# Kernel optimization log

Measured on AMD Instinct MI355X. Metric: run time of the kernel, lower is better.

## Reference

```python
import jax, jax.numpy as jnp
import numpy as np
import math

B, ENC, SEQ, H = 32, 512, 1024, 8
HD = SEQ // H  # 128
EPS = 1e-5


def setup_inputs() -> dict:
    key = jax.random.key(0)
    ks = jax.random.split(key, 7)
    s = 0.02
    return {
        "x": jax.random.normal(ks[0], (B, ENC, SEQ), jnp.float32),
        "ln_g": jnp.ones((SEQ,), jnp.float32),
        "ln_b": jnp.zeros((SEQ,), jnp.float32),
        "w_in": jax.random.normal(ks[1], (3 * SEQ, SEQ), jnp.float32) * s,
        "b_in": jnp.zeros((3 * SEQ,), jnp.float32),
        "w_m1a": jax.random.normal(ks[2], (HD, HD), jnp.float32) * s,
        "b_m1a": jnp.zeros((HD,), jnp.float32),
        "w_m1b": jax.random.normal(ks[3], (1, HD), jnp.float32) * s,
        "b_m1b": jnp.zeros((1,), jnp.float32),
        "w_m2": jax.random.normal(ks[4], (1, ENC), jnp.float32) * s,
        "b_m2": jnp.zeros((1,), jnp.float32),
        "w_out": jax.random.normal(ks[5], (SEQ, 2 * SEQ), jnp.float32) * s,
        "b_out": jnp.zeros((SEQ,), jnp.float32),
    }


def reference(x, ln_g, ln_b, w_in, b_in, w_m1a, b_m1a, w_m1b, b_m1b,
              w_m2, b_m2, w_out, b_out):
    Bsz, N, S = x.shape  # N == enc_in, S == seq_len == d_model
    hd = S // H
    scale = 1.0 / math.sqrt(hd * N)

    # LayerNorm over last dim
    mu = jnp.mean(x, axis=-1, keepdims=True)
    var = jnp.mean(jnp.square(x - mu), axis=-1, keepdims=True)
    xn = (x - mu) * jax.lax.rsqrt(var + EPS) * ln_g + ln_b

    qkv = xn @ w_in.T + b_in  # [B, N, 3S]
    q, k, v = jnp.split(qkv, 3, axis=-1)
    # torch .view(B, H, N, hd) on contiguous [B, N, S] is a raw reshape
    q = q.reshape(Bsz, H, N, hd)
    k = k.reshape(Bsz, H, N, hd)
    v = v.reshape(Bsz, H, N, hd)

    def mlp1(t):  # [B,H,N,hd] -> [B,H,N]
        h1 = jnp.maximum(jnp.einsum('bhnd,ed->bhne', t, w_m1a) + b_m1a, 0.0)
        return jnp.einsum('bhne,e->bhn', h1, w_m1b[0]) + b_m1b[0]

    def mlp2(t):  # [B,H,N,hd] -> [B,H,hd] (Linear over N then ReLU)
        return jnp.maximum(jnp.einsum('bhnd,n->bhd', t, w_m2[0]) + b_m2[0], 0.0)

    # rank-1 outer-product scores, broadcast-multiplied into v
    s_qk = mlp1(q)[..., None] * mlp2(k)[:, :, None, :] * scale  # [B,H,N,hd]
    v1 = (s_qk * v).reshape(Bsz, N, S)
    s_kq = mlp1(k)[..., None] * mlp2(q)[:, :, None, :] * scale
    v2 = (s_kq * v).reshape(Bsz, N, S)

    out = jnp.concatenate([v1, v2], axis=-1) @ w_out.T + b_out  # [B,N,S]
    return out + x  # dropout is identity at eval
```

## Files before the change

kernel.cpp:

```cpp
#include <hip/hip_runtime.h>
#include <cstdint>
#include <cstddef>

#define BSZ   32
#define ENCN  512
#define SEQL  1024
#define MROWS (BSZ*ENCN)
#define N1    (3*SEQL)
#define K1    SEQL
#define N2    SEQL
#define K2    (2*SEQL)

typedef __bf16 bf16;
typedef __bf16 bf16x8 __attribute__((ext_vector_type(8)));
typedef __bf16 bf16x4 __attribute__((ext_vector_type(4)));
typedef float  f32x4  __attribute__((ext_vector_type(4)));
typedef int    i32x4  __attribute__((ext_vector_type(4)));
typedef int    i32x8  __attribute__((ext_vector_type(8)));

__device__ __forceinline__ void gl_lds16(const void* g, void* l) {
  __builtin_amdgcn_global_load_lds(
      (const __attribute__((address_space(1))) void*)(uintptr_t)g,
      (__attribute__((address_space(3))) void*)(uintptr_t)(uint32_t)(uintptr_t)l,
      16, 0, 0);
}

__device__ __forceinline__ f32x4 mfma16(bf16x8 a, bf16x8 b, f32x4 c) {
  return __builtin_amdgcn_mfma_f32_16x16x32_bf16(a, b, c, 0, 0, 0);
}

__device__ __forceinline__ uint32_t pk4_fp8(float a, float b, float c, float d) {
  int v = __builtin_amdgcn_cvt_pk_fp8_f32(a, b, 0, false);
  v = __builtin_amdgcn_cvt_pk_fp8_f32(c, d, v, true);
  return (uint32_t)v;
}

__global__ __launch_bounds__(256) void cvt_w_kernel(const float* __restrict__ w_in,
                                                    const float* __restrict__ w_out,
                                                    const float* __restrict__ w1a,
                                                    uint8_t* __restrict__ wi8,
                                                    uint8_t* __restrict__ wo8,
                                                    bf16* __restrict__ w1ab) {
  int idx = blockIdx.x * 256 + threadIdx.x;
  const int NWIN4 = (N1 * K1) / 4;
  const int NOUT4 = (N2 * K2) / 4;
  if (idx < NWIN4) {
    float4 v = ((const float4*)w_in)[idx];
    ((uint32_t*)wi8)[idx] = pk4_fp8(v.x * 64.f, v.y * 64.f, v.z * 64.f, v.w * 64.f);
  } else if (idx < NWIN4 + NOUT4) {
    int j = idx - NWIN4;
    float4 v = ((const float4*)w_out)[j];
    ((uint32_t*)wo8)[j] = pk4_fp8(v.x * 64.f, v.y * 64.f, v.z * 64.f, v.w * 64.f);
  } else {
    int j = idx - NWIN4 - NOUT4;
    float4 v = ((const float4*)w1a)[j];
    bf16x4 o = { (bf16)v.x, (bf16)v.y, (bf16)v.z, (bf16)v.w };
    ((bf16x4*)w1ab)[j] = o;
  }
}

__global__ __launch_bounds__(256) void ln_kernel(const float* __restrict__ x,
                                                 const float* __restrict__ g,
                                                 const float* __restrict__ bt,
                                                 uint8_t* __restrict__ xn8) {
  int row = blockIdx.x;
  int t = threadIdx.x;
  const float4 v = ((const float4*)(x + (size_t)row * SEQL))[t];
  float s  = v.x + v.y + v.z + v.w;
  float ss = v.x*v.x + v.y*v.y + v.z*v.z + v.w*v.w;
  for (int off = 32; off; off >>= 1) {
    s  += __shfl_down(s,  off, 64);
    ss += __shfl_down(ss, off, 64);
  }
  __shared__ float red[8];
  int w = t >> 6, l = t & 63;
  if (l == 0) { red[w] = s; red[w + 4] = ss; }
  __syncthreads();
  float st  = red[0] + red[1] + red[2] + red[3];
  float sst = red[4] + red[5] + red[6] + red[7];
  float mu   = st * (1.0f / SEQL);
  float var  = sst * (1.0f / SEQL) - mu * mu;
  float rstd = rsqrtf(var + 1e-5f);
  float4 gv = ((const float4*)g)[t];
  float4 bv = ((const float4*)bt)[t];
  float y0 = (v.x - mu) * rstd * gv.x + bv.x;
  float y1 = (v.y - mu) * rstd * gv.y + bv.y;
  float y2 = (v.z - mu) * rstd * gv.z + bv.z;
  float y3 = (v.w - mu) * rstd * gv.w + bv.w;
  ((uint32_t*)(xn8 + (size_t)row * SEQL))[t] = pk4_fp8(y0, y1, y2, y3);
}

template <int MODE, int SA, int SB>
__global__ __launch_bounds__(256) void gemm_fp8(const uint8_t* __restrict__ A,
                                                const uint8_t* __restrict__ Bw,
                                                const float* __restrict__ bias,
                                                const float* __restrict__ resid,
                                                void* __restrict__ Cout,
                                                int M, int N, int K) {
  __shared__ uint8_t Als[128 * 128];
  __shared__ uint8_t Bls[128 * 128];
  const int tid = threadIdx.x;
  const int w = tid >> 6, l = tid & 63;
  const int wm = w & 1, wn = w >> 1;
  const int q = l >> 4, li = l & 15;
  const int m0 = blockIdx.x * 128;
  const int n0 = blockIdx.y * 128;

  const int srow = tid >> 3;
  const int scol = ((tid & 7) ^ (srow & 7)) << 4;

  const int c0 = ((2 * q)     ^ (li & 7)) << 4;
  const int c1 = ((2 * q + 1) ^ (li & 7)) << 4;

  f32x4 acc[4][4] = {};

  for (int k0 = 0; k0 < K; k0 += 128) {
#pragma unroll
    for (int is = 0; is < 4; is++) {
      gl_lds16(A  + (size_t)(m0 + is * 32 + srow) * K + k0 + scol,
               (char*)Als + is * 4096 + w * 1024);
      gl_lds16(Bw + (size_t)(n0 + is * 32 + srow) * K + k0 + scol,
               (char*)Bls + is * 4096 + w * 1024);
    }
    __syncthreads();
    i32x8 af[4], bfg[4];
#pragma unroll
    for (int i = 0; i < 4; i++) {
      int r = wm * 64 + i * 16 + li;
      i32x4 lo = *(const i32x4*)&Als[r * 128 + c0];
      i32x4 hi = *(const i32x4*)&Als[r * 128 + c1];
      af[i] = i32x8{lo[0], lo[1], lo[2], lo[3], hi[0], hi[1], hi[2], hi[3]};
    }
#pragma unroll
    for (int j = 0; j < 4; j++) {
      int r = wn * 64 + j * 16 + li;
      i32x4 lo = *(const i32x4*)&Bls[r * 128 + c0];
      i32x4 hi = *(const i32x4*)&Bls[r * 128 + c1];
      bfg[j] = i32x8{lo[0], lo[1], lo[2], lo[3], hi[0], hi[1], hi[2], hi[3]};
    }
#pragma unroll
    for (int i = 0; i < 4; i++)
#pragma unroll
      for (int j = 0; j < 4; j++)
        acc[i][j] = __builtin_amdgcn_mfma_scale_f32_16x16x128_f8f6f4(
            af[i], bfg[j], acc[i][j], 0 , 0 ,
            0, SA, 0, SB);
    __syncthreads();
  }

#pragma unroll
  for (int i = 0; i < 4; i++)
#pragma unroll
    for (int j = 0; j < 4; j++) {
      int col = n0 + wn * 64 + j * 16 + li;
      float bv = bias[col];
#pragma unroll
      for (int r = 0; r < 4; r++) {
        int row = m0 + wm * 64 + i * 16 + q * 4 + r;
        float v = acc[i][j][r] + bv;
        if (MODE == 0) {
          ((bf16*)Cout)[(size_t)row * N + col] = (bf16)v;
        } else {
          ((float*)Cout)[(size_t)row * N + col] = v + resid[(size_t)row * N + col];
        }
      }
    }
}

__global__ __launch_bounds__(256) void mlp1_kernel(const bf16* __restrict__ qkv,
                                                   const bf16* __restrict__ w1ab,
                                                   const float* __restrict__ b1a,
                                                   const float* __restrict__ w1b,
                                                   const float* __restrict__ b1b,
                                                   float* __restrict__ A1q,
                                                   float* __restrict__ A1k) {
  const int bid = blockIdx.x;
  const int tensor = bid >> 10;
  const int mtile = bid & 1023;
  const int tid = threadIdx.x;
  const int w = tid >> 6, l = tid & 63;
  const int wm = w & 1, wn = w >> 1;
  const int q = l >> 4, li = l & 15;

  bf16x8 bfrag[4][4];
#pragma unroll
  for (int kq = 0; kq < 4; kq++)
#pragma unroll
    for (int j = 0; j < 4; j++) {
      int n = wn * 64 + j * 16 + li;
      bfrag[kq][j] = *(const bf16x8*)&w1ab[n * 128 + kq * 32 + q * 8];
    }

  f32x4 acc[4][4] = {};
#pragma unroll
  for (int kq = 0; kq < 4; kq++) {
#pragma unroll
    for (int i = 0; i < 4; i++) {
      int cg = mtile * 128 + wm * 64 + i * 16 + li;
      int b = cg >> 12;
      int c = cg & 4095;
      const bf16* ap = qkv + (size_t)(b * 512 + (c >> 3)) * N1
                           + tensor * 1024 + (c & 7) * 128 + kq * 32 + q * 8;
      bf16x8 af = *(const bf16x8*)ap;
#pragma unroll
      for (int j = 0; j < 4; j++)
        acc[i][j] = mfma16(af, bfrag[kq][j], acc[i][j]);
    }
  }

  float b1av[4], w1bv[4];
#pragma unroll
  for (int j = 0; j < 4; j++) {
    int col = wn * 64 + j * 16 + li;
    b1av[j] = b1a[col];
    w1bv[j] = w1b[col];
  }
  __shared__ float red[2][128];
  float p[4][4];
#pragma unroll
  for (int i = 0; i < 4; i++)
#pragma unroll
    for (int r = 0; r < 4; r++) {
      float s = 0.f;
#pragma unroll
      for (int j = 0; j < 4; j++) {
        float h = acc[i][j][r] + b1av[j];
        s += fmaxf(h, 0.f) * w1bv[j];
      }
      for (int off = 1; off < 16; off <<= 1) s += __shfl_xor(s, off, 64);
      p[i][r] = s;
    }
  if (li == 0) {
#pragma unroll
    for (int i = 0; i < 4; i++)
#pragma unroll
      for (int r = 0; r < 4; r++)
        red[wn][wm * 64 + i * 16 + q * 4 + r] = p[i][r];
  }
  __syncthreads();
  if (tid < 128) {
    float v = red[0][tid] + red[1][tid] + b1b[0];
    float* outp = tensor ? A1k : A1q;
    outp[mtile * 128 + tid] = v;
  }
}

__global__ __launch_bounds__(256) void mlp2_kernel(const bf16* __restrict__ qkv,
                                                   const float* __restrict__ w2,
                                                   const float* __restrict__ b2,
                                                   float* __restrict__ A2q,
                                                   float* __restrict__ A2k) {
  __shared__ float w2s[512];
  __shared__ float red[256][8];
  const int bid = blockIdx.x;
  const int tensor = bid >> 8;
  const int bh = bid & 255;
  const int b = bh >> 3, h = bh & 7;
  const int t = threadIdx.x;
  w2s[t] = w2[t];
  w2s[t + 256] = w2[t + 256];
  __syncthreads();

  const int half = t >> 7, cg = t & 127;
  const bf16* base = qkv + (size_t)(b * 512 + h * 64) * N1 + tensor * 1024 + cg * 8;
  float acc[8] = {0, 0, 0, 0, 0, 0, 0, 0};
  for (int rr = half; rr < 64; rr += 2) {
    bf16x8 v = *(const bf16x8*)(base + (size_t)rr * N1);
    float wn = w2s[rr * 8 + (cg >> 4)];
#pragma unroll
    for (int e = 0; e < 8; e++) acc[e] += (float)v[e] * wn;
  }
#pragma unroll
  for (int e = 0; e < 8; e++) red[t][e] = acc[e];
  __syncthreads();
  if (t < 128) {
    int m = t >> 3, e = t & 7;
    float s = 0.f;
#pragma unroll
    for (int a = 0; a < 8; a++)
      s += red[a * 16 + m][e] + red[128 + a * 16 + m][e];
    s += b2[0];
    float* o = tensor ? A2k : A2q;
    o[b * 1024 + h * 128 + t] = fmaxf(s, 0.f);
  }
}

__global__ __launch_bounds__(256) void scale_kernel(const bf16* __restrict__ qkv,
                                                    const float* __restrict__ A1q,
                                                    const float* __restrict__ A1k,
                                                    const float* __restrict__ A2q,
                                                    const float* __restrict__ A2k,
                                                    uint8_t* __restrict__ Y) {
  size_t idx = ((size_t)blockIdx.x * 256 + threadIdx.x) * 8;
  int b = (int)(idx >> 19);
  int f = (int)(idx & 524287);
  int chunk = f >> 7;
  float a1q = A1q[b * 4096 + chunk] * 64.f;
  float a1k = A1k[b * 4096 + chunk] * 64.f;
  int a2i = b * 1024 + ((f >> 16) << 7) + (f & 127);
  float4 k0 = *(const float4*)&A2k[a2i];
  float4 k1 = *(const float4*)&A2k[a2i + 4];
  float4 q0 = *(const float4*)&A2q[a2i];
  float4 q1 = *(const float4*)&A2q[a2i + 4];
  int row = b * 512 + (f >> 10);
  int col = f & 1023;
  bf16x8 v = *(const bf16x8*)&qkv[(size_t)row * N1 + 2048 + col];
  float kk[8] = { k0.x, k0.y, k0.z, k0.w, k1.x, k1.y, k1.z, k1.w };
  float qq[8] = { q0.x, q0.y, q0.z, q0.w, q1.x, q1.y, q1.z, q1.w };
  float y1[8], y2[8];
#pragma unroll
  for (int e = 0; e < 8; e++) {
    float vv = (float)v[e];
    y1[e] = a1q * kk[e] * vv;
    y2[e] = a1k * qq[e] * vv;
  }
  uint8_t* yr = Y + (size_t)row * K2;
  ((uint32_t*)(yr + col))[0] = pk4_fp8(y1[0], y1[1], y1[2], y1[3]);
  ((uint32_t*)(yr + col))[1] = pk4_fp8(y1[4], y1[5], y1[6], y1[7]);
  ((uint32_t*)(yr + 1024 + col))[0] = pk4_fp8(y2[0], y2[1], y2[2], y2[3]);
  ((uint32_t*)(yr + 1024 + col))[1] = pk4_fp8(y2[4], y2[5], y2[6], y2[7]);
}

extern "C" void kernel_launch(void* const* d_in, const int* in_sizes, int n_in,
                              void* d_out, int out_size, void* d_ws, size_t ws_size,
                              hipStream_t stream) {
  const float* x     = (const float*)d_in[0];
  const float* ln_g  = (const float*)d_in[1];
  const float* ln_b  = (const float*)d_in[2];
  const float* w_in  = (const float*)d_in[3];
  const float* b_in  = (const float*)d_in[4];
  const float* w1a   = (const float*)d_in[5];
  const float* b1a   = (const float*)d_in[6];
  const float* w1b   = (const float*)d_in[7];
  const float* b1b   = (const float*)d_in[8];
  const float* w2    = (const float*)d_in[9];
  const float* b2    = (const float*)d_in[10];
  const float* w_out = (const float*)d_in[11];
  const float* b_out = (const float*)d_in[12];
  float* out = (float*)d_out;
  char* ws = (char*)d_ws;

  uint8_t* xn8  = (uint8_t*)(ws);
  bf16*    qkv  = (bf16*)   (ws + 16777216);
  uint8_t* Y8   = (uint8_t*)(ws + 117440512);
  uint8_t* wi8  = (uint8_t*)(ws + 150994944);
  uint8_t* wo8  = (uint8_t*)(ws + 154140672);
  bf16*    w1ab = (bf16*)   (ws + 156237824);
  float*   A1q  = (float*)  (ws + 156270592);
  float*   A1k  = (float*)  (ws + 156794880);
  float*   A2q  = (float*)  (ws + 157319168);
  float*   A2k  = (float*)  (ws + 157450240);

  cvt_w_kernel<<<5136, 256, 0, stream>>>(w_in, w_out, w1a, wi8, wo8, w1ab);
  ln_kernel<<<MROWS, 256, 0, stream>>>(x, ln_g, ln_b, xn8);
  gemm_fp8<0, 127, 121><<<dim3(MROWS / 128, N1 / 128), 256, 0, stream>>>(
      xn8, wi8, b_in, nullptr, qkv, MROWS, N1, K1);
  mlp1_kernel<<<2048, 256, 0, stream>>>(qkv, w1ab, b1a, w1b, b1b, A1q, A1k);
  mlp2_kernel<<<512, 256, 0, stream>>>(qkv, w2, b2, A2q, A2k);
  scale_kernel<<<8192, 256, 0, stream>>>(qkv, A1q, A1k, A2q, A2k, Y8);
  gemm_fp8<1, 113, 121><<<dim3(MROWS / 128, N2 / 128), 256, 0, stream>>>(
      Y8, wo8, b_out, x, out, MROWS, N2, K2);
}
```

Before: 320.3 us.

## Fuse mlp1, mlp2 and scale kernels into one per-head attention kernel

Replaces three separate kernels with one kernel where each block handles one (batch, head) group. It computes the mlp1 scores, the mlp2 reduction and the scaled fp8 output using shared memory instead of global A1/A2 buffers. This removes two launches and the global round trips of the intermediate vectors. In exchange, only 256 large blocks run, with serialized phases and many barriers, which may reduce latency hiding.

```diff
diff --git a/kernel.cpp b/kernel.cpp
--- a/kernel.cpp
+++ b/kernel.cpp
@@ -167,158 +167,117 @@
     }
 }
 
-__global__ __launch_bounds__(256) void mlp1_kernel(const bf16* __restrict__ qkv,
-                                                   const bf16* __restrict__ w1ab,
-                                                   const float* __restrict__ b1a,
-                                                   const float* __restrict__ w1b,
-                                                   const float* __restrict__ b1b,
-                                                   float* __restrict__ A1q,
-                                                   float* __restrict__ A1k) {
-  const int bid = blockIdx.x;
-  const int tensor = bid >> 10;
-  const int mtile = bid & 1023;
+__global__ __launch_bounds__(512) void attn_fused(const bf16* __restrict__ qkv,
+                                                  const bf16* __restrict__ w1ab,
+                                                  const float* __restrict__ b1a,
+                                                  const float* __restrict__ w1b,
+                                                  const float* __restrict__ b1b,
+                                                  const float* __restrict__ w2,
+                                                  const float* __restrict__ b2,
+                                                  uint8_t* __restrict__ Y) {
+  __shared__ float A1s[2][512];
+  __shared__ float A2s[2][128];
+  __shared__ float red1[2][256];
+  __shared__ float redm[512][8];
+  __shared__ float w2s[512];
   const int tid = threadIdx.x;
   const int w = tid >> 6, l = tid & 63;
-  const int wm = w & 1, wn = w >> 1;
+  const int wm = w & 3, wn = w >> 2;
   const int q = l >> 4, li = l & 15;
+  const int R0 = blockIdx.x * 64;
+  const bf16* qbase = qkv + (size_t)R0 * N1;
+
+  w2s[tid] = w2[tid];
 
   bf16x8 bfrag[4][4];
-#pragma unroll
-  for (int kq = 0; kq < 4; kq++)
-#pragma unroll
-    for (int j = 0; j < 4; j++) {
-      int n = wn * 64 + j * 16 + li;
+  float b1av[4], w1bv[4];
+#pragma unroll
+  for (int j = 0; j < 4; j++) {
+    int n = wn * 64 + j * 16 + li;
+#pragma unroll
+    for (int kq = 0; kq < 4; kq++)
       bfrag[kq][j] = *(const bf16x8*)&w1ab[n * 128 + kq * 32 + q * 8];
-    }
-
-  f32x4 acc[4][4] = {};
-#pragma unroll
-  for (int kq = 0; kq < 4; kq++) {
-#pragma unroll
-    for (int i = 0; i < 4; i++) {
-      int cg = mtile * 128 + wm * 64 + i * 16 + li;
-      int b = cg >> 12;
-      int c = cg & 4095;
-      const bf16* ap = qkv + (size_t)(b * 512 + (c >> 3)) * N1
-                           + tensor * 1024 + (c & 7) * 128 + kq * 32 + q * 8;
-      bf16x8 af = *(const bf16x8*)ap;
-#pragma unroll
-      for (int j = 0; j < 4; j++)
-        acc[i][j] = mfma16(af, bfrag[kq][j], acc[i][j]);
-    }
-  }
-
-  float b1av[4], w1bv[4];
-#pragma unroll
-  for (int j = 0; j < 4; j++) {
-    int col = wn * 64 + j * 16 + li;
-    b1av[j] = b1a[col];
-    w1bv[j] = w1b[col];
-  }
-  __shared__ float red[2][128];
-  float p[4][4];
-#pragma unroll
-  for (int i = 0; i < 4; i++)
-#pragma unroll
-    for (int r = 0; r < 4; r++) {
-      float s = 0.f;
-#pragma unroll
-      for (int j = 0; j < 4; j++) {
-        float h = acc[i][j][r] + b1av[j];
-        s += fmaxf(h, 0.f) * w1bv[j];
+    b1av[j] = b1a[n];
+    w1bv[j] = w1b[n];
+  }
+  const float b1b0 = b1b[0], b2_0 = b2[0];
+
+  for (int T = 0; T < 2; T++) {
+    for (int p = 0; p < 2; p++) {
+      f32x4 acc[4][4] = {};
+#pragma unroll
+      for (int kq = 0; kq < 4; kq++) {
+#pragma unroll
+        for (int i = 0; i < 4; i++) {
+          int n = p * 256 + wm * 64 + i * 16 + li;
+          bf16x8 af = *(const bf16x8*)(qbase + (size_t)(n >> 3) * N1
+                                       + T * 1024 + (n & 7) * 128 + kq * 32 + q * 8);
+#pragma unroll
+          for (int j = 0; j < 4; j++)
+            acc[i][j] = mfma16(af, bfrag[kq][j], acc[i][j]);
+        }
       }
-      for (int off = 1; off < 16; off <<= 1) s += __shfl_xor(s, off, 64);
-      p[i][r] = s;
-    }
-  if (li == 0) {
-#pragma unroll
-    for (int i = 0; i < 4; i++)
-#pragma unroll
-      for (int r = 0; r < 4; r++)
-        red[wn][wm * 64 + i * 16 + q * 4 + r] = p[i][r];
-  }
-  __syncthreads();
-  if (tid < 128) {
-    float v = red[0][tid] + red[1][tid] + b1b[0];
-    float* outp = tensor ? A1k : A1q;
-    outp[mtile * 128 + tid] = v;
-  }
-}
-
-__global__ __launch_bounds__(256) void mlp2_kernel(const bf16* __restrict__ qkv,
-                                                   const float* __restrict__ w2,
-                                                   const float* __restrict__ b2,
-                                                   float* __restrict__ A2q,
-                                                   float* __restrict__ A2k) {
-  __shared__ float w2s[512];
-  __shared__ float red[256][8];
-  const int bid = blockIdx.x;
-  const int tensor = bid >> 8;
-  const int bh = bid & 255;
-  const int b = bh >> 3, h = bh & 7;
-  const int t = threadIdx.x;
-  w2s[t] = w2[t];
-  w2s[t + 256] = w2[t + 256];
-  __syncthreads();
-
-  const int half = t >> 7, cg = t & 127;
-  const bf16* base = qkv + (size_t)(b * 512 + h * 64) * N1 + tensor * 1024 + cg * 8;
-  float acc[8] = {0, 0, 0, 0, 0, 0, 0, 0};
-  for (int rr = half; rr < 64; rr += 2) {
-    bf16x8 v = *(const bf16x8*)(base + (size_t)rr * N1);
-    float wn = w2s[rr * 8 + (cg >> 4)];
-#pragma unroll
-    for (int e = 0; e < 8; e++) acc[e] += (float)v[e] * wn;
-  }
-#pragma unroll
-  for (int e = 0; e < 8; e++) red[t][e] = acc[e];
-  __syncthreads();
-  if (t < 128) {
-    int m = t >> 3, e = t & 7;
-    float s = 0.f;
-#pragma unroll
-    for (int a = 0; a < 8; a++)
-      s += red[a * 16 + m][e] + red[128 + a * 16 + m][e];
-    s += b2[0];
-    float* o = tensor ? A2k : A2q;
-    o[b * 1024 + h * 128 + t] = fmaxf(s, 0.f);
-  }
-}
-
-__global__ __launch_bounds__(256) void scale_kernel(const bf16* __restrict__ qkv,
-                                                    const float* __restrict__ A1q,
-                                                    const float* __restrict__ A1k,
-                                                    const float* __restrict__ A2q,
-                                                    const float* __restrict__ A2k,
-                                                    uint8_t* __restrict__ Y) {
-  size_t idx = ((size_t)blockIdx.x * 256 + threadIdx.x) * 8;
-  int b = (int)(idx >> 19);
-  int f = (int)(idx & 524287);
-  int chunk = f >> 7;
-  float a1q = A1q[b * 4096 + chunk] * 64.f;
-  float a1k = A1k[b * 4096 + chunk] * 64.f;
-  int a2i = b * 1024 + ((f >> 16) << 7) + (f & 127);
-  float4 k0 = *(const float4*)&A2k[a2i];
-  float4 k1 = *(const float4*)&A2k[a2i + 4];
-  float4 q0 = *(const float4*)&A2q[a2i];
-  float4 q1 = *(const float4*)&A2q[a2i + 4];
-  int row = b * 512 + (f >> 10);
-  int col = f & 1023;
-  bf16x8 v = *(const bf16x8*)&qkv[(size_t)row * N1 + 2048 + col];
-  float kk[8] = { k0.x, k0.y, k0.z, k0.w, k1.x, k1.y, k1.z, k1.w };
-  float qq[8] = { q0.x, q0.y, q0.z, q0.w, q1.x, q1.y, q1.z, q1.w };
-  float y1[8], y2[8];
-#pragma unroll
-  for (int e = 0; e < 8; e++) {
-    float vv = (float)v[e];
-    y1[e] = a1q * kk[e] * vv;
-    y2[e] = a1k * qq[e] * vv;
-  }
-  uint8_t* yr = Y + (size_t)row * K2;
-  ((uint32_t*)(yr + col))[0] = pk4_fp8(y1[0], y1[1], y1[2], y1[3]);
-  ((uint32_t*)(yr + col))[1] = pk4_fp8(y1[4], y1[5], y1[6], y1[7]);
-  ((uint32_t*)(yr + 1024 + col))[0] = pk4_fp8(y2[0], y2[1], y2[2], y2[3]);
-  ((uint32_t*)(yr + 1024 + col))[1] = pk4_fp8(y2[4], y2[5], y2[6], y2[7]);
+#pragma unroll
+      for (int i = 0; i < 4; i++)
+#pragma unroll
+        for (int r = 0; r < 4; r++) {
+          float s = 0.f;
+#pragma unroll
+          for (int j = 0; j < 4; j++)
+            s += fmaxf(acc[i][j][r] + b1av[j], 0.f) * w1bv[j];
+          for (int off = 1; off < 16; off <<= 1) s += __shfl_xor(s, off, 64);
+          if (li == 0) red1[wn][wm * 64 + i * 16 + q * 4 + r] = s;
+        }
+      __syncthreads();
+      if (tid < 256) A1s[T][p * 256 + tid] = red1[0][tid] + red1[1][tid] + b1b0;
+      __syncthreads();
+    }
+    {
+      const int qu = tid >> 7, cg8 = tid & 127;
+      const bf16* base = qbase + T * 1024 + cg8 * 8;
+      float a8[8] = {0, 0, 0, 0, 0, 0, 0, 0};
+      for (int rr = qu; rr < 64; rr += 4) {
+        bf16x8 v = *(const bf16x8*)(base + (size_t)rr * N1);
+        float wgt = w2s[rr * 8 + (cg8 >> 4)];
+#pragma unroll
+        for (int e = 0; e < 8; e++) a8[e] += (float)v[e] * wgt;
+      }
+#pragma unroll
+      for (int e = 0; e < 8; e++) redm[tid][e] = a8[e];
+      __syncthreads();
+      if (tid < 128) {
+        float s = 0.f;
+#pragma unroll
+        for (int qu2 = 0; qu2 < 4; qu2++)
+#pragma unroll
+          for (int cb = 0; cb < 8; cb++)
+            s += redm[qu2 * 128 + cb * 16 + (tid >> 3)][tid & 7];
+        A2s[T][tid] = fmaxf(s + b2_0, 0.f);
+      }
+      __syncthreads();
+    }
+  }
+
+  for (int it = 0; it < 16; it++) {
+    int g = it * 512 + tid;
+    int row_l = g >> 7, colg = g & 127, col = colg * 8;
+    int n = row_l * 8 + (colg >> 4);
+    bf16x8 v = *(const bf16x8*)(qbase + (size_t)row_l * N1 + 2048 + col);
+    float a1q64 = A1s[0][n] * 64.f, a1k64 = A1s[1][n] * 64.f;
+    int d0 = col & 127;
+    float y1[8], y2[8];
+#pragma unroll
+    for (int e = 0; e < 8; e++) {
+      float vv = (float)v[e];
+      y1[e] = a1q64 * A2s[1][d0 + e] * vv;
+      y2[e] = a1k64 * A2s[0][d0 + e] * vv;
+    }
+    uint8_t* yr = Y + (size_t)(R0 + row_l) * K2;
+    ((uint32_t*)(yr + col))[0] = pk4_fp8(y1[0], y1[1], y1[2], y1[3]);
+    ((uint32_t*)(yr + col))[1] = pk4_fp8(y1[4], y1[5], y1[6], y1[7]);
+    ((uint32_t*)(yr + 1024 + col))[0] = pk4_fp8(y2[0], y2[1], y2[2], y2[3]);
+    ((uint32_t*)(yr + 1024 + col))[1] = pk4_fp8(y2[4], y2[5], y2[6], y2[7]);
+  }
 }
 
 extern "C" void kernel_launch(void* const* d_in, const int* in_sizes, int n_in,
@@ -346,18 +305,12 @@
   uint8_t* wi8  = (uint8_t*)(ws + 150994944);
   uint8_t* wo8  = (uint8_t*)(ws + 154140672);
   bf16*    w1ab = (bf16*)   (ws + 156237824);
-  float*   A1q  = (float*)  (ws + 156270592);
-  float*   A1k  = (float*)  (ws + 156794880);
-  float*   A2q  = (float*)  (ws + 157319168);
-  float*   A2k  = (float*)  (ws + 157450240);
 
   cvt_w_kernel<<<5136, 256, 0, stream>>>(w_in, w_out, w1a, wi8, wo8, w1ab);
   ln_kernel<<<MROWS, 256, 0, stream>>>(x, ln_g, ln_b, xn8);
   gemm_fp8<0, 127, 121><<<dim3(MROWS / 128, N1 / 128), 256, 0, stream>>>(
       xn8, wi8, b_in, nullptr, qkv, MROWS, N1, K1);
-  mlp1_kernel<<<2048, 256, 0, stream>>>(qkv, w1ab, b1a, w1b, b1b, A1q, A1k);
-  mlp2_kernel<<<512, 256, 0, stream>>>(qkv, w2, b2, A2q, A2k);
-  scale_kernel<<<8192, 256, 0, stream>>>(qkv, A1q, A1k, A2q, A2k, Y8);
+  attn_fused<<<256, 512, 0, stream>>>(qkv, w1ab, b1a, w1b, b1b, w2, b2, Y8);
   gemm_fp8<1, 113, 121><<<dim3(MROWS / 128, N2 / 128), 256, 0, stream>>>(
       Y8, wo8, b_out, x, out, MROWS, N2, K2);
 }
```

Measured after the change: 319.4 us. About the same (-0.3%).

## Fuse mlp1 and mlp2 into one kernel sharing q/k tile reads

Applied to the files above, without the earlier changes.

Merges the per-row MLP1 kernel and the column-reduction MLP2 kernel into a single kernel. Each block covers 16 rows of one (batch, head) for q or k, computes the MLP1 outputs with MFMA and the partial MLP2 sums over the same tile, then writes per-quarter partials. A small a2c kernel adds the four partials, the bias and the ReLU. The point is to read the q/k part of the qkv buffer once instead of twice, at the cost of an extra launch and a partial-sum buffer.

```diff
diff --git a/kernel.cpp b/kernel.cpp
--- a/kernel.cpp
+++ b/kernel.cpp
@@ -167,122 +167,104 @@
     }
 }
 
-__global__ __launch_bounds__(256) void mlp1_kernel(const bf16* __restrict__ qkv,
-                                                   const bf16* __restrict__ w1ab,
-                                                   const float* __restrict__ b1a,
-                                                   const float* __restrict__ w1b,
-                                                   const float* __restrict__ b1b,
-                                                   float* __restrict__ A1q,
-                                                   float* __restrict__ A1k) {
+__global__ __launch_bounds__(256) void mlp12_kernel(const bf16* __restrict__ qkv,
+                                                    const bf16* __restrict__ w1ab,
+                                                    const float* __restrict__ b1a,
+                                                    const float* __restrict__ w1b,
+                                                    const float* __restrict__ b1b,
+                                                    const float* __restrict__ w2,
+                                                    float* __restrict__ A1q,
+                                                    float* __restrict__ A1k,
+                                                    float* __restrict__ A2p) {
+  __shared__ float red1[2][128];
+  __shared__ float redm[16][128];
+  __shared__ float w2s[128];
   const int bid = blockIdx.x;
-  const int tensor = bid >> 10;
-  const int mtile = bid & 1023;
+  const int T = bid >> 10;
+  const int rem = bid & 1023;
+  const int bh = rem >> 2, quarter = rem & 3;
   const int tid = threadIdx.x;
   const int w = tid >> 6, l = tid & 63;
   const int wm = w & 1, wn = w >> 1;
   const int q = l >> 4, li = l & 15;
+  const int R0 = bh * 64 + quarter * 16;
+  const bf16* rbase = qkv + (size_t)R0 * N1 + T * 1024;
+
+  if (tid < 128) w2s[tid] = w2[quarter * 128 + tid];
 
   bf16x8 bfrag[4][4];
-#pragma unroll
-  for (int kq = 0; kq < 4; kq++)
-#pragma unroll
-    for (int j = 0; j < 4; j++) {
-      int n = wn * 64 + j * 16 + li;
+  float b1av[4], w1bv[4];
+#pragma unroll
+  for (int j = 0; j < 4; j++) {
+    int n = wn * 64 + j * 16 + li;
+#pragma unroll
+    for (int kq = 0; kq < 4; kq++)
       bfrag[kq][j] = *(const bf16x8*)&w1ab[n * 128 + kq * 32 + q * 8];
-    }
+    b1av[j] = b1a[n];
+    w1bv[j] = w1b[n];
+  }
 
   f32x4 acc[4][4] = {};
 #pragma unroll
   for (int kq = 0; kq < 4; kq++) {
 #pragma unroll
     for (int i = 0; i < 4; i++) {
-      int cg = mtile * 128 + wm * 64 + i * 16 + li;
-      int b = cg >> 12;
-      int c = cg & 4095;
-      const bf16* ap = qkv + (size_t)(b * 512 + (c >> 3)) * N1
-                           + tensor * 1024 + (c & 7) * 128 + kq * 32 + q * 8;
-      bf16x8 af = *(const bf16x8*)ap;
+      int lc = wm * 64 + i * 16 + li;
+      bf16x8 af = *(const bf16x8*)(rbase + (size_t)(lc >> 3) * N1
+                                   + (lc & 7) * 128 + kq * 32 + q * 8);
 #pragma unroll
       for (int j = 0; j < 4; j++)
         acc[i][j] = mfma16(af, bfrag[kq][j], acc[i][j]);
     }
   }
-
-  float b1av[4], w1bv[4];
-#pragma unroll
-  for (int j = 0; j < 4; j++) {
-    int col = wn * 64 + j * 16 + li;
-    b1av[j] = b1a[col];
-    w1bv[j] = w1b[col];
-  }
-  __shared__ float red[2][128];
-  float p[4][4];
 #pragma unroll
   for (int i = 0; i < 4; i++)
 #pragma unroll
     for (int r = 0; r < 4; r++) {
       float s = 0.f;
 #pragma unroll
-      for (int j = 0; j < 4; j++) {
-        float h = acc[i][j][r] + b1av[j];
-        s += fmaxf(h, 0.f) * w1bv[j];
-      }
+      for (int j = 0; j < 4; j++)
+        s += fmaxf(acc[i][j][r] + b1av[j], 0.f) * w1bv[j];
       for (int off = 1; off < 16; off <<= 1) s += __shfl_xor(s, off, 64);
-      p[i][r] = s;
-    }
-  if (li == 0) {
-#pragma unroll
-    for (int i = 0; i < 4; i++)
-#pragma unroll
-      for (int r = 0; r < 4; r++)
-        red[wn][wm * 64 + i * 16 + q * 4 + r] = p[i][r];
-  }
+      if (li == 0) red1[wn][wm * 64 + i * 16 + q * 4 + r] = s;
+    }
   __syncthreads();
   if (tid < 128) {
-    float v = red[0][tid] + red[1][tid] + b1b[0];
-    float* outp = tensor ? A1k : A1q;
-    outp[mtile * 128 + tid] = v;
-  }
-}
-
-__global__ __launch_bounds__(256) void mlp2_kernel(const bf16* __restrict__ qkv,
-                                                   const float* __restrict__ w2,
-                                                   const float* __restrict__ b2,
-                                                   float* __restrict__ A2q,
-                                                   float* __restrict__ A2k) {
-  __shared__ float w2s[512];
-  __shared__ float red[256][8];
-  const int bid = blockIdx.x;
-  const int tensor = bid >> 8;
-  const int bh = bid & 255;
-  const int b = bh >> 3, h = bh & 7;
-  const int t = threadIdx.x;
-  w2s[t] = w2[t];
-  w2s[t + 256] = w2[t + 256];
+    float v = red1[0][tid] + red1[1][tid] + b1b[0];
+    (T ? A1k : A1q)[bh * 512 + quarter * 128 + tid] = v;
+  }
+
+  const int rg = tid >> 4, dg = tid & 15;
+  const bf16* arow = rbase + (size_t)rg * N1 + dg * 8;
+  float a8[8] = {0, 0, 0, 0, 0, 0, 0, 0};
+#pragma unroll
+  for (int cc = 0; cc < 8; cc++) {
+    bf16x8 v = *(const bf16x8*)(arow + cc * 128);
+    float wgt = w2s[rg * 8 + cc];
+#pragma unroll
+    for (int e = 0; e < 8; e++) a8[e] += (float)v[e] * wgt;
+  }
+#pragma unroll
+  for (int e = 0; e < 8; e++) redm[rg][dg * 8 + e] = a8[e];
   __syncthreads();
-
-  const int half = t >> 7, cg = t & 127;
-  const bf16* base = qkv + (size_t)(b * 512 + h * 64) * N1 + tensor * 1024 + cg * 8;
-  float acc[8] = {0, 0, 0, 0, 0, 0, 0, 0};
-  for (int rr = half; rr < 64; rr += 2) {
-    bf16x8 v = *(const bf16x8*)(base + (size_t)rr * N1);
-    float wn = w2s[rr * 8 + (cg >> 4)];
-#pragma unroll
-    for (int e = 0; e < 8; e++) acc[e] += (float)v[e] * wn;
-  }
-#pragma unroll
-  for (int e = 0; e < 8; e++) red[t][e] = acc[e];
-  __syncthreads();
-  if (t < 128) {
-    int m = t >> 3, e = t & 7;
+  if (tid < 128) {
     float s = 0.f;
 #pragma unroll
-    for (int a = 0; a < 8; a++)
-      s += red[a * 16 + m][e] + red[128 + a * 16 + m][e];
-    s += b2[0];
-    float* o = tensor ? A2k : A2q;
-    o[b * 1024 + h * 128 + t] = fmaxf(s, 0.f);
-  }
+    for (int rg2 = 0; rg2 < 16; rg2++) s += redm[rg2][tid];
+    A2p[(((size_t)T * 256 + bh) * 4 + quarter) * 128 + tid] = s;
+  }
+}
+
+__global__ __launch_bounds__(256) void a2c_kernel(const float* __restrict__ A2p,
+                                                  const float* __restrict__ b2,
+                                                  float* __restrict__ A2q,
+                                                  float* __restrict__ A2k) {
+  int idx = blockIdx.x * 256 + threadIdx.x;
+  int t = idx >> 15, r = idx & 32767;
+  int bh = r >> 7, d = r & 127;
+  const float* p = A2p + ((size_t)t * 256 + bh) * 512 + d;
+  float s = p[0] + p[128] + p[256] + p[384] + b2[0];
+  (t ? A2k : A2q)[r] = fmaxf(s, 0.f);
 }
 
 __global__ __launch_bounds__(256) void scale_kernel(const bf16* __restrict__ qkv,
@@ -348,15 +330,16 @@
   bf16*    w1ab = (bf16*)   (ws + 156237824);
   float*   A1q  = (float*)  (ws + 156270592);
   float*   A1k  = (float*)  (ws + 156794880);
-  float*   A2q  = (float*)  (ws + 157319168);
-  float*   A2k  = (float*)  (ws + 157450240);
+  float*   A2p  = (float*)  (ws + 157319168);
+  float*   A2q  = (float*)  (ws + 158367744);
+  float*   A2k  = (float*)  (ws + 158498816);
 
   cvt_w_kernel<<<5136, 256, 0, stream>>>(w_in, w_out, w1a, wi8, wo8, w1ab);
   ln_kernel<<<MROWS, 256, 0, stream>>>(x, ln_g, ln_b, xn8);
   gemm_fp8<0, 127, 121><<<dim3(MROWS / 128, N1 / 128), 256, 0, stream>>>(
       xn8, wi8, b_in, nullptr, qkv, MROWS, N1, K1);
-  mlp1_kernel<<<2048, 256, 0, stream>>>(qkv, w1ab, b1a, w1b, b1b, A1q, A1k);
-  mlp2_kernel<<<512, 256, 0, stream>>>(qkv, w2, b2, A2q, A2k);
+  mlp12_kernel<<<2048, 256, 0, stream>>>(qkv, w1ab, b1a, w1b, b1b, w2, A1q, A1k, A2p);
+  a2c_kernel<<<256, 256, 0, stream>>>(A2p, b2, A2q, A2k);
   scale_kernel<<<8192, 256, 0, stream>>>(qkv, A1q, A1k, A2q, A2k, Y8);
   gemm_fp8<1, 113, 121><<<dim3(MROWS / 128, N2 / 128), 256, 0, stream>>>(
       Y8, wo8, b_out, x, out, MROWS, N2, K2);
```

Result: no change. 324.0 us (+1.2%).
